# Performance work log

Measured on AMD Instinct MI355X. Metric: run time of the kernel, lower is better.

Reference implementation:

```python
import jax, jax.numpy as jnp
import numpy as np

N_QUBITS = 16
BATCH = 512
NUM_CLASSES = 100


def _rx_mat(theta):
    """RX matrix; theta shape (...,) -> (..., 2, 2) complex64."""
    c = jnp.cos(theta / 2).astype(jnp.complex64)
    s = (-1j * jnp.sin(theta / 2)).astype(jnp.complex64)
    row0 = jnp.stack([c, s], axis=-1)
    row1 = jnp.stack([s, c], axis=-1)
    return jnp.stack([row0, row1], axis=-2)


def _rot_mat(phi, theta, omega):
    """qml.Rot = RZ(omega) RY(theta) RZ(phi); scalars/arrays -> (..., 2, 2)."""
    c = jnp.cos(theta / 2)
    s = jnp.sin(theta / 2)
    e_m = jnp.exp(-0.5j * (phi + omega).astype(jnp.complex64))
    e_p = jnp.exp(0.5j * (phi + omega).astype(jnp.complex64))
    e_dm = jnp.exp(-0.5j * (phi - omega).astype(jnp.complex64))
    e_dp = jnp.exp(0.5j * (phi - omega).astype(jnp.complex64))
    row0 = jnp.stack([e_m * c, -e_dp * s], axis=-1)
    row1 = jnp.stack([e_dm * s, e_p * c], axis=-1)
    return jnp.stack([row0, row1], axis=-2).astype(jnp.complex64)


def _apply_1q(state, U, w):
    """Apply shared (2,2) gate U on wire w. state: (B,) + (2,)*16."""
    s = jnp.moveaxis(state, w + 1, -1)
    s = jnp.einsum('ij,...j->...i', U, s)
    return jnp.moveaxis(s, -1, w + 1)


def _apply_1q_batched(state, U, w):
    """Apply per-sample (B,2,2) gate on wire w."""
    s = jnp.moveaxis(state, w + 1, -1)
    s = jnp.einsum('bij,b...j->b...i', U, s)
    return jnp.moveaxis(s, -1, w + 1)


def _apply_crx(state, theta, ctrl, tgt):
    """Controlled-RX(theta) with control ctrl, target tgt (shared scalar theta)."""
    U = _rx_mat(theta)
    s = jnp.moveaxis(state, (ctrl + 1, tgt + 1), (-2, -1))
    s1 = jnp.einsum('ij,...j->...i', U, s[..., 1, :])
    s = jnp.stack([s[..., 0, :], s1], axis=-2)
    return jnp.moveaxis(s, (-2, -1), (ctrl + 1, tgt + 1))


def _circuit(x, rot_l1, crx_l1, rot_l2, crx_l2):
    B = x.shape[0]
    # |0...0> initial state, shape (B, 2, 2, ..., 2)
    state = jnp.zeros((B,) + (2,) * N_QUBITS, dtype=jnp.complex64)
    state = state.at[(slice(None),) + (0,) * N_QUBITS].set(1.0)

    for layer_rot, layer_crx in ((rot_l1, crx_l1), (rot_l2, crx_l2)):
        # AngleEmbedding: RX(x[:, i]) on wire i (per-sample angles)
        for i in range(N_QUBITS):
            state = _apply_1q_batched(state, _rx_mat(x[:, i]), i)
        # Rot gates
        for i in range(N_QUBITS):
            U = _rot_mat(layer_rot[i, 0], layer_rot[i, 1], layer_rot[i, 2])
            state = _apply_1q(state, U, i)
        # ring CRX
        for i in range(N_QUBITS):
            state = _apply_crx(state, layer_crx[i, 0], i, (i + 1) % N_QUBITS)

    # <Z_i> = P(bit_i = 0) - P(bit_i = 1)
    probs = state.real ** 2 + state.imag ** 2  # (B,) + (2,)*16
    expvals = []
    for i in range(N_QUBITS):
        axes = tuple(a for a in range(1, N_QUBITS + 1) if a != i + 1)
        marg = probs.sum(axis=axes)  # (B, 2)
        expvals.append(marg[:, 0] - marg[:, 1])
    return jnp.stack(expvals, axis=1).astype(jnp.float32)  # (B, 16)


def setup_inputs() -> dict:
    key = jax.random.key(0)
    ks = jax.random.split(key, 7)
    return {
        'x': jax.random.normal(ks[0], (BATCH, N_QUBITS), jnp.float32),
        'rot_l1': jax.random.normal(ks[1], (N_QUBITS, 3), jnp.float32),
        'crx_l1': jax.random.normal(ks[2], (N_QUBITS, 1), jnp.float32),
        'rot_l2': jax.random.normal(ks[3], (N_QUBITS, 3), jnp.float32),
        'crx_l2': jax.random.normal(ks[4], (N_QUBITS, 1), jnp.float32),
        'W': jax.random.normal(ks[5], (NUM_CLASSES, N_QUBITS), jnp.float32) * 0.25,
        'b': jax.random.normal(ks[6], (NUM_CLASSES,), jnp.float32) * 0.01,
    }


def reference(x, rot_l1, crx_l1, rot_l2, crx_l2, W, b):
    feats = _circuit(x, rot_l1, crx_l1, rot_l2, crx_l2)  # (B, 16)
    logits = feats @ W.T + b  # (B, num_classes)
    return jax.nn.log_softmax(logits, axis=1)
```

## Files before the change

### kernel.cpp

```cpp
#include <hip/hip_runtime.h>
#include <math.h>

#define NQ 16
#define NBATCH 512
#define NCLS 100

typedef float v2f __attribute__((ext_vector_type(2)));
typedef __fp16 f16x2 __attribute__((ext_vector_type(2)));
typedef _Float16 half8 __attribute__((ext_vector_type(8)));
typedef float f32x4 __attribute__((ext_vector_type(4)));

__device__ __forceinline__ v2f mkv(float x, float y){ v2f r; r.x = x; r.y = y; return r; }
__device__ __forceinline__ f16x2 pack_h(v2f a){ return __builtin_amdgcn_cvt_pkrtz(a.x, a.y); }
__device__ __forceinline__ f16x2 pack_h2(float a, float b){ return __builtin_amdgcn_cvt_pkrtz(a, b); }
__device__ __forceinline__ v2f unpack_h(f16x2 h){ return mkv((float)h.x, (float)h.y); }

union pack16 { f16x2 h[4]; uint4 u; };

__device__ __forceinline__ v2f pk_cmul(v2f a, v2f b){
  v2f t, d;
  asm("v_pk_mul_f32 %0, %1, %2 op_sel:[0,0] op_sel_hi:[1,0]"
      : "=v"(t) : "v"(a), "v"(b));
  asm("v_pk_fma_f32 %0, %1, %2, %3 op_sel:[1,1,0] op_sel_hi:[0,1,1] neg_lo:[1,0,0]"
      : "=v"(d) : "v"(a), "v"(b), "v"(t));
  return d;
}
__device__ __forceinline__ v2f pk_cmul_acc(v2f a, v2f b, v2f acc){
  v2f t, d;
  asm("v_pk_fma_f32 %0, %1, %2, %3 op_sel:[0,0,0] op_sel_hi:[1,0,1]"
      : "=v"(t) : "v"(a), "v"(b), "v"(acc));
  asm("v_pk_fma_f32 %0, %1, %2, %3 op_sel:[1,1,0] op_sel_hi:[0,1,1] neg_lo:[1,0,0]"
      : "=v"(d) : "v"(a), "v"(b), "v"(t));
  return d;
}
__device__ __forceinline__ void pk_rx(v2f &a, v2f &b, v2f cs){
  v2f t1, t2, na, nb;
  asm("v_pk_mul_f32 %0, %1, %2 op_sel:[0,0] op_sel_hi:[0,1]"
      : "=v"(t1) : "v"(cs), "v"(a));
  asm("v_pk_mul_f32 %0, %1, %2 op_sel:[0,0] op_sel_hi:[0,1]"
      : "=v"(t2) : "v"(cs), "v"(b));
  asm("v_pk_fma_f32 %0, %1, %2, %3 op_sel:[1,1,0] op_sel_hi:[1,0,1] neg_hi:[0,1,0]"
      : "=v"(na) : "v"(cs), "v"(b), "v"(t1));
  asm("v_pk_fma_f32 %0, %1, %2, %3 op_sel:[1,1,0] op_sel_hi:[1,0,1] neg_hi:[0,1,0]"
      : "=v"(nb) : "v"(cs), "v"(a), "v"(t2));
  a = na; b = nb;
}

template<int MT>
__device__ __forceinline__ void crx_pred(v2f (&v)[16], bool on, v2f cs){
  v2f id = mkv(1.f, 0.f);
  v2f cs_p = on ? cs : id;
  #pragma unroll
  for (int r=0;r<16;r++) if(!(r&MT)) pk_rx(v[r], v[r|MT], cs_p);
}
template<int MT>
__device__ __forceinline__ void crx_on(v2f (&v)[16], v2f cs){
  #pragma unroll
  for (int r=0;r<16;r++) if(!(r&MT)) pk_rx(v[r], v[r|MT], cs);
}
template<int MC,int MT>
__device__ __forceinline__ void crx_rr(v2f (&v)[16], v2f cs){
  #pragma unroll
  for (int r=0;r<16;r++) if((r&MC)&&!(r&MT)) pk_rx(v[r], v[r|MT], cs);
}
template<int M>
__device__ __forceinline__ void reg_gate(v2f (&v)[16], v2f u00, v2f u01, v2f u10, v2f u11){
  #pragma unroll
  for (int r=0;r<16;r++) if(!(r&M)){
    v2f a = v[r], b = v[r|M];
    v[r]   = pk_cmul_acc(u01, b, pk_cmul(u00, a));
    v[r|M] = pk_cmul_acc(u11, b, pk_cmul(u10, a));
  }
}
__device__ __forceinline__ void build_rxw(v2f cs, v2f w00, v2f w01, v2f w10, v2f w11,
      v2f &f00, v2f &f01, v2f &f10, v2f &f11){
  f00 = w00; f10 = w10; pk_rx(f00, f10, cs);
  f01 = w01; f11 = w11; pk_rx(f01, f11, cs);
}

__device__ __forceinline__ int lds_phys(int c){ return c ^ (((c>>4)^(c>>8))&15); }
__device__ __forceinline__ int swz(int m, int q){
  return m*4 + (q ^ (m&3) ^ ((m>>2)&3));
}
__device__ __forceinline__ int oswz(int idx){ return idx ^ ((idx>>5)&31); }

__global__ __launch_bounds__(256) void kprep(const float* __restrict__ x,
      const float* __restrict__ rot1, const float* __restrict__ crx1,
      const float* __restrict__ rot2, const float* __restrict__ crx2,
      v2f* __restrict__ fU, v2f* __restrict__ cm)
{
  int t = blockIdx.x*blockDim.x + threadIdx.x;
  if (t < 2*NBATCH*NQ){
    int w  = t & 15;
    int bb = (t>>4) & (NBATCH-1);
    int L  = t >> 13;
    const float* rot = L ? rot2 : rot1;
    float phi = rot[w*3+0], th = rot[w*3+1], om = rot[w*3+2];
    float ct = cosf(0.5f*th), stt = sinf(0.5f*th);
    float a1 = 0.5f*(phi+om), a2 = 0.5f*(phi-om);
    float emx = cosf(a1), emy = -sinf(a1);
    float epx = cosf(a1), epy =  sinf(a1);
    float edmx = cosf(a2), edmy = -sinf(a2);
    float edpx = cosf(a2), edpy =  sinf(a2);
    float R00x = emx*ct,   R00y = emy*ct;
    float R01x = -edpx*stt, R01y = -edpy*stt;
    float R10x = edmx*stt, R10y = edmy*stt;
    float R11x = epx*ct,   R11y = epy*ct;
    float xv = x[bb*NQ + w];
    float cx = cosf(0.5f*xv), sx = sinf(0.5f*xv);
    v2f* o = fU + (size_t)t*4;
    o[0] = mkv(R00x*cx + R01y*sx,  R00y*cx - R01x*sx);
    o[1] = mkv(R00y*sx + R01x*cx, -R00x*sx + R01y*cx);
    o[2] = mkv(R10x*cx + R11y*sx,  R10y*cx - R11x*sx);
    o[3] = mkv(R10y*sx + R11x*cx, -R10x*sx + R11y*cx);
  }
  if (t < 2*NQ){
    int L = t>>4, w = t&15;
    const float* cxl = L ? crx2 : crx1;
    float thc = cxl[w];
    cm[t] = mkv(cosf(0.5f*thc), sinf(0.5f*thc));
  }
}

__global__ __launch_bounds__(256) void kprep2(const v2f* __restrict__ fU,
      const v2f* __restrict__ cm, v2f* __restrict__ Tbl)
{
  int t = blockIdx.x*blockDim.x + threadIdx.x;
  if (t >= 2*NBATCH) return;
  int bb = t >> 1, bit = t & 1;
  const v2f* U = fU + (size_t)bb*64;
  v2f p[16];
  p[0] = U[48]; p[1] = U[50];
  p[2] = pk_cmul(p[0], U[54]); p[3] = pk_cmul(p[1], U[54]);
  p[0] = pk_cmul(p[0], U[52]); p[1] = pk_cmul(p[1], U[52]);
  #pragma unroll
  for (int i=0;i<4;i++){ p[i+4]=pk_cmul(p[i],U[58]); p[i]=pk_cmul(p[i],U[56]); }
  #pragma unroll
  for (int i=0;i<8;i++){ p[i+8]=pk_cmul(p[i],U[62]); p[i]=pk_cmul(p[i],U[60]); }
  if (bit){
    #pragma unroll
    for (int r=0;r<16;r++) if(!(r&1)) pk_rx(p[r], p[r|1], cm[11]);
  }
  #pragma unroll
  for (int r=0;r<16;r++) if((r&1)&&!(r&2)) pk_rx(p[r], p[r|2], cm[12]);
  #pragma unroll
  for (int r=0;r<16;r++) if((r&2)&&!(r&4)) pk_rx(p[r], p[r|4], cm[13]);
  #pragma unroll
  for (int r=0;r<16;r++) if((r&4)&&!(r&8)) pk_rx(p[r], p[r|8], cm[14]);
  v2f* o = Tbl + ((size_t)bb<<5) + (bit<<4);
  #pragma unroll
  for (int r=0;r<16;r++) o[r] = p[r];
}

__device__ __forceinline__ void store_Bfrag(_Float16* Bt16, size_t hb, int r0, const v2f (&v)[16]){
  int k0 = 2*r0;
  int lk = 16*(k0>>3);
  int j0 = k0 & 7;
  #pragma unroll
  for (int n=0;n<16;n++){
    _Float16 re  = (_Float16)v[n].x;
    _Float16 im  = (_Float16)v[n].y;
    _Float16 nim = (_Float16)(-v[n].y);
    size_t ln = (size_t)(lk + n);
    Bt16[((hb+0)*64 + ln)*8 + j0]   = re;
    Bt16[((hb+0)*64 + ln)*8 + j0+1] = nim;
    Bt16[((hb+1)*64 + ln)*8 + j0]   = im;
    Bt16[((hb+1)*64 + ln)*8 + j0+1] = re;
  }
}

__global__ __launch_bounds__(256) void kprepG(const v2f* __restrict__ fU2,
      const v2f* __restrict__ cm2, _Float16* __restrict__ Bt16)
{
  int t = blockIdx.x*blockDim.x + threadIdx.x;
  if (t >= NBATCH*2*2*16) return;
  int r0 = t & 15;
  int var = (t>>4) & 1;
  int stage = (t>>5) & 1;
  int bg = t >> 6;
  const v2f* U2 = fU2 + ((size_t)bg<<6);
  v2f v[16];
  #pragma unroll
  for (int r=0;r<16;r++) v[r] = mkv(0.f,0.f);
  v[r0] = mkv(1.f,0.f);
  if (stage == 0){
    reg_gate<1>(v, U2[28],U2[29],U2[30],U2[31]);
    reg_gate<2>(v, U2[32],U2[33],U2[34],U2[35]);
    reg_gate<4>(v, U2[36],U2[37],U2[38],U2[39]);
    reg_gate<8>(v, U2[40],U2[41],U2[42],U2[43]);
    if (var) crx_on<1>(v, cm2[6]);
    crx_rr<1,2>(v, cm2[7]);
    crx_rr<2,4>(v, cm2[8]);
    crx_rr<4,8>(v, cm2[9]);
  } else {
    reg_gate<1>(v, U2[44],U2[45],U2[46],U2[47]);
    reg_gate<2>(v, U2[48],U2[49],U2[50],U2[51]);
    reg_gate<4>(v, U2[52],U2[53],U2[54],U2[55]);
    reg_gate<8>(v, U2[56],U2[57],U2[58],U2[59]);
    if (var) crx_on<1>(v, cm2[10]);
    crx_rr<1,2>(v, cm2[11]);
    crx_rr<2,4>(v, cm2[12]);
    crx_rr<4,8>(v, cm2[13]);
  }
  size_t hb = (((size_t)bg*2 + stage)*2 + var)*2;
  store_Bfrag(Bt16, hb, r0, v);
}

__global__ __launch_bounds__(256) void kprepG2(const v2f* __restrict__ fU2,
      const v2f* __restrict__ cm1, const v2f* __restrict__ cm2,
      _Float16* __restrict__ Bt16)
{
  int t = blockIdx.x*blockDim.x + threadIdx.x;
  if (t >= NBATCH*2*2*16) return;
  int r0 = t & 15;
  int var = (t>>4) & 1;
  int stage = (t>>5) & 1;
  int bg = t >> 6;
  const v2f* U2 = fU2 + ((size_t)bg<<6);
  v2f v[16];
  #pragma unroll
  for (int r=0;r<16;r++) v[r] = mkv(0.f,0.f);
  v[r0] = mkv(1.f,0.f);
  if (stage == 0){
    if (var) crx_on<1>(v, cm1[15]);
    reg_gate<1>(v, U2[0], U2[1], U2[2], U2[3]);
    reg_gate<2>(v, U2[4], U2[5], U2[6], U2[7]);
    reg_gate<4>(v, U2[8], U2[9], U2[10],U2[11]);
    reg_gate<8>(v, U2[12],U2[13],U2[14],U2[15]);
    crx_rr<1,2>(v, cm2[0]);
    crx_rr<2,4>(v, cm2[1]);
    crx_rr<4,8>(v, cm2[2]);
  } else {
    reg_gate<1>(v, U2[16],U2[17],U2[18],U2[19]);
    reg_gate<2>(v, U2[20],U2[21],U2[22],U2[23]);
    reg_gate<4>(v, U2[24],U2[25],U2[26],U2[27]);
    if (var) crx_on<1>(v, cm2[3]);
    crx_rr<1,2>(v, cm2[4]);
    crx_rr<2,4>(v, cm2[5]);
  }
  size_t hb = (((size_t)bg*2 + stage)*2 + var)*2;
  store_Bfrag(Bt16, hb, r0, v);
}

__global__ __launch_bounds__(256) void kpass1(const v2f* __restrict__ fU1,
      const v2f* __restrict__ cm1, f16x2* __restrict__ compact)
{
  int lane = threadIdx.x & 63;
  int wv = threadIdx.x >> 6;
  int bg = blockIdx.x;
  const v2f* U = fU1 + ((size_t)bg<<6);
  v2f a = (lane&1) ? U[2] : U[0];
  a = pk_cmul(a, ((lane>>1)&1) ? U[22] : U[20]);
  a = pk_cmul(a, ((lane>>2)&1) ? U[26] : U[24]);
  a = pk_cmul(a, ((lane>>3)&1) ? U[30] : U[28]);
  a = pk_cmul(a, ((lane>>4)&1) ? U[34] : U[32]);
  a = pk_cmul(a, ((lane>>5)&1) ? U[38] : U[36]);
  a = pk_cmul(a, (wv&1) ? U[42] : U[40]);
  a = pk_cmul(a, ((wv>>1)&1) ? U[46] : U[44]);
  v2f v[16];
  v[0] = pk_cmul(a, U[4]);    v[1] = pk_cmul(a, U[6]);
  v[2] = pk_cmul(v[0], U[10]); v[3] = pk_cmul(v[1], U[10]);
  v[0] = pk_cmul(v[0], U[8]);  v[1] = pk_cmul(v[1], U[8]);
  #pragma unroll
  for (int i=0;i<4;i++){ v[i+4]=pk_cmul(v[i],U[14]); v[i]=pk_cmul(v[i],U[12]); }
  #pragma unroll
  for (int i=0;i<8;i++){ v[i+8]=pk_cmul(v[i],U[18]); v[i]=pk_cmul(v[i],U[16]); }
  crx_pred<1>(v, (lane&1)!=0, cm1[0]);
  crx_rr<1,2>(v, cm1[1]);
  crx_rr<2,4>(v, cm1[2]);
  crx_rr<4,8>(v, cm1[3]);
  __shared__ v2f lds[4096];
  #pragma unroll
  for (int r=0;r<16;r++){
    int c = (lane&1) | (r<<1) | (((lane>>1)&31)<<5) | (wv<<10);
    lds[lds_phys(c)] = v[r];
  }
  __syncthreads();
  #pragma unroll
  for (int r=0;r<16;r++){
    int c = ((lane>>1)&15) | ((lane&1)<<4) | (r<<5) | (((lane>>5)&1)<<9) | (wv<<10);
    v[r] = lds[lds_phys(c)];
  }
  crx_pred<1>(v, (lane&1)!=0, cm1[4]);
  crx_rr<1,2>(v, cm1[5]);
  crx_rr<2,4>(v, cm1[6]);
  crx_rr<4,8>(v, cm1[7]);
  __syncthreads();
  #pragma unroll
  for (int r=0;r<16;r++){
    int c = ((lane>>1)&15) | ((lane&1)<<4) | (r<<5) | (((lane>>5)&1)<<9) | (wv<<10);
    lds[lds_phys(c)] = v[r];
  }
  __syncthreads();
  #pragma unroll
  for (int r=0;r<16;r++){
    int c = (lane&63) | (wv<<6) | (((r>>3)&1)<<8) | ((r&7)<<9);
    v[r] = lds[lds_phys(c)];
  }
  crx_rr<8,1>(v, cm1[8]);
  crx_rr<1,2>(v, cm1[9]);
  crx_rr<2,4>(v, cm1[10]);
  __syncthreads();
  #pragma unroll
  for (int r=0;r<16;r++){
    int c = (lane&63) | (wv<<6) | (((r>>3)&1)<<8) | ((r&7)<<9);
    lds[lds_phys(c)] = v[r];
  }
  __syncthreads();
  f16x2* outp = compact + ((size_t)bg<<12);
  #pragma unroll
  for (int r=0;r<16;r++){
    int c = ((lane>>1)&31) | (wv<<5) | (r<<7) | ((lane&1)<<11);
    outp[lane | (wv<<6) | (r<<8)] = pack_h(lds[lds_phys(c)]);
  }
}

__global__ __launch_bounds__(256) void kpass2(const f16x2* __restrict__ compact,
      const v2f* __restrict__ Tbl, const half8* __restrict__ Btab2,
      f16x2* __restrict__ st, int b0)
{
  int lane = threadIdx.x & 63;
  int wv = threadIdx.x >> 6;
  int blk = blockIdx.x;
  int bl = blk >> 4, h = blk & 15;
  int bg = b0 + bl;
  __shared__ uint4 lbufA[1024];
  __shared__ uint4 lbufB[1024];
  f16x2* lbufH = (f16x2*)lbufA;

  v2f a = unpack_h(compact[((size_t)bg<<12) | (size_t)(lane | (wv<<6) | (h<<8))]);
  const v2f* T = Tbl + ((size_t)bg<<5) + ((lane&1)<<4);
  int sel = wv & 1;
  size_t hb1 = (((size_t)bg*2 + 0)*2 + sel)*2;
  size_t hb2 = (((size_t)bg*2 + 1)*2 + sel)*2;
  half8 B1a = Btab2[(hb1+0)*64 + lane];
  half8 B2a = Btab2[(hb1+1)*64 + lane];
  half8 B1b = Btab2[(hb2+0)*64 + lane];
  half8 B2b = Btab2[(hb2+1)*64 + lane];
  f32x4 zz = {0.f, 0.f, 0.f, 0.f};

  int kb = (lane>>1) & 15;
  int mA_fix = (lane&1) | ((lane>>5)<<4) | ((wv&1)<<5) | ((wv>>1)<<7);
  #pragma unroll
  for (int r=0;r<16;r++){
    v2f val = pk_cmul(a, T[r]);
    int m = mA_fix | ((r&7)<<1) | ((r>>3)<<6);
    lbufH[swz(m, kb>>2)*4 + (kb&3)] = pack_h(val);
  }
  __syncthreads();

  f32x4 dre[4], dim[4];
  #pragma unroll
  for (int t=0;t<4;t++){
    int m = (wv<<6) | (t<<4) | (lane&15);
    half8 af = *(const half8*)&lbufA[swz(m, lane>>4)];
    dre[t] = __builtin_amdgcn_mfma_f32_16x16x32_f16(af, B1a, zz, 0, 0, 0);
    dim[t] = __builtin_amdgcn_mfma_f32_16x16x32_f16(af, B2a, zz, 0, 0, 0);
  }
  int n = lane & 15, lq = lane >> 4;
  int q_c = ((wv>>1)&1) | ((n&1)<<1);
  #pragma unroll
  for (int reg=0;reg<4;reg++){
    int mC = (lq&1) | (((n>>1)&1)<<1) | (((n>>2)&1)<<2) | ((lq>>1)<<3)
           | ((reg&1)<<4) | (((reg>>1)&1)<<5) | (((n>>3)&1)<<6) | ((wv&1)<<7);
    pack16 pk;
    #pragma unroll
    for (int t=0;t<4;t++) pk.h[t] = pack_h2(dre[t][reg], dim[t][reg]);
    lbufB[swz(mC, q_c)] = pk.u;
  }
  __syncthreads();

  #pragma unroll
  for (int t2=0;t2<4;t2++){
    int m = (wv<<6) | (t2<<4) | (lane&15);
    half8 af = *(const half8*)&lbufB[swz(m, lane>>4)];
    f32x4 ere = __builtin_amdgcn_mfma_f32_16x16x32_f16(af, B1b, zz, 0, 0, 0);
    f32x4 eim = __builtin_amdgcn_mfma_f32_16x16x32_f16(af, B2b, zz, 0, 0, 0);
    #pragma unroll
    for (int reg=0;reg<4;reg++){
      int idx = ((lane>>3)&1) | (((reg>>1)&1)<<1) | ((t2&1)<<2) | (((t2>>1)&1)<<3)
              | ((reg&1)<<4) | ((wv&1)<<5) | (((lane>>4)&1)<<6) | (((lane>>5)&1)<<7)
              | ((lane&1)<<8) | (((lane>>1)&1)<<9) | (((lane>>2)&1)<<10) | (((wv>>1)&1)<<11);
      lbufH[oswz(idx)] = pack_h2(ere[reg], eim[reg]);
    }
  }
  __syncthreads();

  f16x2* S = st + ((size_t)bl<<16);
  #pragma unroll
  for (int r=0;r<16;r++){
    int idx = lane | (wv<<6) | (r<<8);
    S[idx | (h<<12)] = lbufH[oswz(idx)];
  }
}

__global__ __launch_bounds__(256) void kpass3(const f16x2* __restrict__ st,
      const v2f* __restrict__ fU2, const v2f* __restrict__ cm2,
      const half8* __restrict__ Btab,
      float* __restrict__ expv, int b0)
{
  int lane = threadIdx.x & 63;
  int wv = threadIdx.x >> 6;
  int blk = blockIdx.x;
  int bl = blk >> 4, h = blk & 15;
  int bg = b0 + bl;
  const f16x2* S = st + ((size_t)bl<<16);
  const v2f* U2 = fU2 + ((size_t)bg<<6);
  __shared__ uint4 lbufA[1024];
  __shared__ uint4 lbufB[1024];

  int abase = (((h>>1)&1)<<5) | ((h&1)<<6) | (((h>>2)&1)<<8) | (((h>>3)&1)<<9)
            | ((wv&1)<<10) | (((wv>>1)&1)<<11);
  f16x2 v[16];
  #pragma unroll
  for (int r=0;r<16;r++){
    v[r] = S[(lane&31) | (((lane>>5)&1)<<7) | abase | (r<<12)];
  }
  int m1 = ((lane>>2)&15) | (((wv>>1)&1)<<4) | ((lane&1)<<5)
         | ((wv&1)<<6) | (((lane>>1)&1)<<7);
  #pragma unroll
  for (int q=0;q<4;q++){
    pack16 pk;
    pk.h[0]=v[4*q]; pk.h[1]=v[4*q+1]; pk.h[2]=v[4*q+2]; pk.h[3]=v[4*q+3];
    lbufA[swz(m1,q)] = pk.u;
  }

  int sel = wv & 1;
  size_t hb1 = (((size_t)bg*2 + 0)*2 + sel)*2;
  size_t hb2 = (((size_t)bg*2 + 1)*2 + sel)*2;
  half8 B1a = Btab[(hb1+0)*64 + lane];
  half8 B2a = Btab[(hb1+1)*64 + lane];
  half8 B1b = Btab[(hb2+0)*64 + lane];
  half8 B2b = Btab[(hb2+1)*64 + lane];
  f32x4 zz = {0.f, 0.f, 0.f, 0.f};

  __syncthreads();

  {
    int n = lane & 15;
    int q2 = lane >> 4;
    #pragma unroll
    for (int t=0;t<4;t++){
      int m = (wv<<6) | (t<<4) | (lane&15);
      half8 af = *(const half8*)&lbufA[swz(m, lane>>4)];
      f32x4 dre = __builtin_amdgcn_mfma_f32_16x16x32_f16(af, B1a, zz, 0, 0, 0);
      f32x4 dim = __builtin_amdgcn_mfma_f32_16x16x32_f16(af, B2a, zz, 0, 0, 0);
      int m2 = t | ((n&7)<<2) | (((wv>>1)&1)<<5) | (((n>>3)&1)<<6) | ((wv&1)<<7);
      pack16 pk;
      #pragma unroll
      for (int rg=0;rg<4;rg++) pk.h[rg] = pack_h2(dre[rg], dim[rg]);
      lbufB[swz(m2, q2)] = pk.u;
    }
  }
  __syncthreads();

  v2f G00, G01, G10, G11;
  {
    v2f g00=U2[60], g01=U2[61], g10=U2[62], g11=U2[63];
    v2f f00,f01,f10,f11;
    build_rxw(cm2[14], g00,g01,g10,g11, f00,f01,f10,f11);
    bool on3 = ((lane>>3)&1) != 0;
    G00 = on3?f00:g00; G01 = on3?f01:g01; G10 = on3?f10:g10; G11 = on3?f11:g11;
  }
  float tot=0.f, S15=0.f, S0w=0.f, S9=0.f, S1w=0.f;
  #pragma unroll
  for (int t2=0;t2<4;t2++){
    int m = (wv<<6) | (t2<<4) | (lane&15);
    half8 af = *(const half8*)&lbufB[swz(m, lane>>4)];
    f32x4 ere = __builtin_amdgcn_mfma_f32_16x16x32_f16(af, B1b, zz, 0, 0, 0);
    f32x4 eim = __builtin_amdgcn_mfma_f32_16x16x32_f16(af, B2b, zz, 0, 0, 0);
    v2f a0 = mkv(ere[0], eim[0]);
    v2f a1 = mkv(ere[1], eim[1]);
    v2f a2 = mkv(ere[2], eim[2]);
    v2f a3 = mkv(ere[3], eim[3]);
    v2f n0 = pk_cmul_acc(G01, a1, pk_cmul(G00, a0));
    v2f n1 = pk_cmul_acc(G11, a1, pk_cmul(G10, a0));
    v2f n2 = pk_cmul_acc(G01, a3, pk_cmul(G00, a2));
    v2f n3 = pk_cmul_acc(G11, a3, pk_cmul(G10, a2));
    pk_rx(n1, n3, cm2[15]);
    float p0 = n0.x*n0.x + n0.y*n0.y;
    float p1 = n1.x*n1.x + n1.y*n1.y;
    float p2 = n2.x*n2.x + n2.y*n2.y;
    float p3 = n3.x*n3.x + n3.y*n3.y;
    float ps = p0+p1+p2+p3;
    tot += ps;
    S15 += p1+p3;
    S0w += p2+p3;
    if (t2&1) S9 += ps;
    if (t2&2) S1w += ps;
  }
  float s = tot;
  float u[6];
  #pragma unroll
  for (int b=0;b<6;b++){
    int m = 1<<b;
    float tt = __shfl_xor(s, m, 64);
    u[b] = s - tt;
    s = s + tt;
    #pragma unroll
    for (int j=0;j<6;j++) if (j<b) u[j] += __shfl_xor(u[j], m, 64);
  }
  #pragma unroll
  for (int d=1; d<64; d<<=1){
    S15 += __shfl_xor(S15, d, 64);
    S0w += __shfl_xor(S0w, d, 64);
    S9  += __shfl_xor(S9, d, 64);
    S1w += __shfl_xor(S1w, d, 64);
  }
  __syncthreads();
  float* ef = (float*)lbufA;
  if (lane==0){
    ef[wv*16+11]=u[0]; ef[wv*16+12]=u[1]; ef[wv*16+13]=u[2]; ef[wv*16+14]=u[3];
    ef[wv*16+7]=u[4];  ef[wv*16+8]=u[5];
    ef[wv*16+15]=s-2.f*S15; ef[wv*16+0]=s-2.f*S0w;
    ef[wv*16+9]=s-2.f*S9;   ef[wv*16+1]=s-2.f*S1w;
    ef[wv*16+10]=(wv&1)?-s:s; ef[wv*16+6]=(wv&2)?-s:s;
    ef[wv*16+2]=(h&1)?-s:s; ef[wv*16+3]=(h&2)?-s:s;
    ef[wv*16+4]=(h&4)?-s:s; ef[wv*16+5]=(h&8)?-s:s;
  }
  __syncthreads();
  if (threadIdx.x < 16){
    float r4 = ef[threadIdx.x]+ef[16+threadIdx.x]+ef[32+threadIdx.x]+ef[48+threadIdx.x];
    atomicAdd(expv + (size_t)bg*NQ + threadIdx.x, r4);
  }
}

__global__ __launch_bounds__(128) void klogits(const float* __restrict__ expv,
      const float* __restrict__ W, const float* __restrict__ bias,
      float* __restrict__ out)
{
  int b = blockIdx.x;
  int tid = threadIdx.x;
  __shared__ float f[NQ];
  __shared__ float lg[NCLS];
  if (tid < NQ) f[tid] = expv[b*NQ + tid];
  __syncthreads();
  if (tid < NCLS){
    float acc = bias[tid];
    #pragma unroll
    for (int i=0;i<NQ;i++) acc += f[i]*W[tid*NQ+i];
    lg[tid] = acc;
  }
  __syncthreads();
  if (tid < NCLS){
    float m = -1e30f;
    for (int i=0;i<NCLS;i++) m = fmaxf(m, lg[i]);
    float sum = 0.f;
    for (int i=0;i<NCLS;i++) sum += expf(lg[i]-m);
    out[b*NCLS+tid] = lg[tid] - m - logf(sum);
  }
}

extern "C" void kernel_launch(void* const* d_in, const int* in_sizes, int n_in,
                              void* d_out, int out_size, void* d_ws, size_t ws_size,
                              hipStream_t stream)
{
  const float* x    = (const float*)d_in[0];
  const float* rot1 = (const float*)d_in[1];
  const float* crx1 = (const float*)d_in[2];
  const float* rot2 = (const float*)d_in[3];
  const float* crx2 = (const float*)d_in[4];
  const float* W    = (const float*)d_in[5];
  const float* bias = (const float*)d_in[6];
  float* out = (float*)d_out;

  char* ws = (char*)d_ws;
  float* expv = (float*)ws;
  v2f*   fU   = (v2f*)(ws + (40<<10));
  v2f*   cmm  = (v2f*)(ws + (560<<10));
  v2f*   Tbl  = (v2f*)(ws + (564<<10));
  _Float16* Bt16  = (_Float16*)(ws + (704<<10));
  _Float16* Bt16b = (_Float16*)(ws + (4800<<10));
  f16x2* compact = (f16x2*)(ws + (8896<<10));
  const size_t stOff = (size_t)(8896<<10) + ((size_t)NBATCH<<14);
  f16x2* st   = (f16x2*)(ws + stOff);

  hipMemsetAsync(expv, 0, NBATCH*NQ*sizeof(float), stream);
  kprep<<<(2*NBATCH*NQ + 255)/256, 256, 0, stream>>>(x, rot1, crx1, rot2, crx2, fU, cmm);

  v2f* fU1 = fU;
  v2f* fU2 = fU + 32768;
  v2f* cm1 = cmm;
  v2f* cm2 = cmm + 16;

  kprep2<<<(2*NBATCH + 255)/256, 256, 0, stream>>>(fU1, cm1, Tbl);
  kprepG<<<(NBATCH*2*2*16 + 255)/256, 256, 0, stream>>>(fU2, cm2, Bt16);
  kprepG2<<<(NBATCH*2*2*16 + 255)/256, 256, 0, stream>>>(fU2, cm1, cm2, Bt16b);
  kpass1<<<NBATCH, 256, 0, stream>>>(fU1, cm1, compact);

  size_t avail = (ws_size > stOff) ? (ws_size - stOff) : 0;
  int chunk = NBATCH;
  while (chunk > 1 && (size_t)chunk*65536*sizeof(f16x2) > avail) chunk >>= 1;

  for (int b0 = 0; b0 < NBATCH; b0 += chunk){
    kpass2<<<chunk*16, 256, 0, stream>>>(compact, Tbl, (const half8*)Bt16b, st, b0);
    kpass3<<<chunk*16, 256, 0, stream>>>(st, fU2, cm2, (const half8*)Bt16, expv, b0);
  }
  klogits<<<NBATCH, 128, 0, stream>>>(expv, W, bias, out);
}
```

Before: 117.6 us.

## Merge gate-prep kernels, halve LDS in pass kernels, defer B-fragment loads

```diff
diff --git a/kernel.cpp b/kernel.cpp
--- a/kernel.cpp
+++ b/kernel.cpp
@@ -31,6 +31,12 @@
       : "=v"(t) : "v"(a), "v"(b), "v"(acc));
   asm("v_pk_fma_f32 %0, %1, %2, %3 op_sel:[1,1,0] op_sel_hi:[0,1,1] neg_lo:[1,0,0]"
       : "=v"(d) : "v"(a), "v"(b), "v"(t));
+  return d;
+}
+__device__ __forceinline__ v2f pk_fma_el(v2f a, v2f b, v2f c){
+  v2f d;
+  asm("v_pk_fma_f32 %0, %1, %2, %3"
+      : "=v"(d) : "v"(a), "v"(b), "v"(c));
   return d;
 }
 __device__ __forceinline__ void pk_rx(v2f &a, v2f &b, v2f cs){
@@ -169,11 +175,13 @@
   }
 }
 
-__global__ __launch_bounds__(256) void kprepG(const v2f* __restrict__ fU2,
-      const v2f* __restrict__ cm2, _Float16* __restrict__ Bt16)
-{
-  int t = blockIdx.x*blockDim.x + threadIdx.x;
-  if (t >= NBATCH*2*2*16) return;
+__global__ __launch_bounds__(256) void kprepGall(const v2f* __restrict__ fU2,
+      const v2f* __restrict__ cm1, const v2f* __restrict__ cm2,
+      _Float16* __restrict__ Bt16, _Float16* __restrict__ Bt16b)
+{
+  int tt = blockIdx.x*blockDim.x + threadIdx.x;
+  int which = tt >> 15;
+  int t = tt & 32767;
   int r0 = t & 15;
   int var = (t>>4) & 1;
   int stage = (t>>5) & 1;
@@ -183,63 +191,49 @@
   #pragma unroll
   for (int r=0;r<16;r++) v[r] = mkv(0.f,0.f);
   v[r0] = mkv(1.f,0.f);
-  if (stage == 0){
-    reg_gate<1>(v, U2[28],U2[29],U2[30],U2[31]);
-    reg_gate<2>(v, U2[32],U2[33],U2[34],U2[35]);
-    reg_gate<4>(v, U2[36],U2[37],U2[38],U2[39]);
-    reg_gate<8>(v, U2[40],U2[41],U2[42],U2[43]);
-    if (var) crx_on<1>(v, cm2[6]);
-    crx_rr<1,2>(v, cm2[7]);
-    crx_rr<2,4>(v, cm2[8]);
-    crx_rr<4,8>(v, cm2[9]);
+  if (which == 0){
+    if (stage == 0){
+      reg_gate<1>(v, U2[28],U2[29],U2[30],U2[31]);
+      reg_gate<2>(v, U2[32],U2[33],U2[34],U2[35]);
+      reg_gate<4>(v, U2[36],U2[37],U2[38],U2[39]);
+      reg_gate<8>(v, U2[40],U2[41],U2[42],U2[43]);
+      if (var) crx_on<1>(v, cm2[6]);
+      crx_rr<1,2>(v, cm2[7]);
+      crx_rr<2,4>(v, cm2[8]);
+      crx_rr<4,8>(v, cm2[9]);
+    } else {
+      reg_gate<1>(v, U2[44],U2[45],U2[46],U2[47]);
+      reg_gate<2>(v, U2[48],U2[49],U2[50],U2[51]);
+      reg_gate<4>(v, U2[52],U2[53],U2[54],U2[55]);
+      reg_gate<8>(v, U2[56],U2[57],U2[58],U2[59]);
+      if (var) crx_on<1>(v, cm2[10]);
+      crx_rr<1,2>(v, cm2[11]);
+      crx_rr<2,4>(v, cm2[12]);
+      crx_rr<4,8>(v, cm2[13]);
+    }
+    size_t hb = (((size_t)bg*2 + stage)*2 + var)*2;
+    store_Bfrag(Bt16, hb, r0, v);
   } else {
-    reg_gate<1>(v, U2[44],U2[45],U2[46],U2[47]);
-    reg_gate<2>(v, U2[48],U2[49],U2[50],U2[51]);
-    reg_gate<4>(v, U2[52],U2[53],U2[54],U2[55]);
-    reg_gate<8>(v, U2[56],U2[57],U2[58],U2[59]);
-    if (var) crx_on<1>(v, cm2[10]);
-    crx_rr<1,2>(v, cm2[11]);
-    crx_rr<2,4>(v, cm2[12]);
-    crx_rr<4,8>(v, cm2[13]);
-  }
-  size_t hb = (((size_t)bg*2 + stage)*2 + var)*2;
-  store_Bfrag(Bt16, hb, r0, v);
-}
-
-__global__ __launch_bounds__(256) void kprepG2(const v2f* __restrict__ fU2,
-      const v2f* __restrict__ cm1, const v2f* __restrict__ cm2,
-      _Float16* __restrict__ Bt16)
-{
-  int t = blockIdx.x*blockDim.x + threadIdx.x;
-  if (t >= NBATCH*2*2*16) return;
-  int r0 = t & 15;
-  int var = (t>>4) & 1;
-  int stage = (t>>5) & 1;
-  int bg = t >> 6;
-  const v2f* U2 = fU2 + ((size_t)bg<<6);
-  v2f v[16];
-  #pragma unroll
-  for (int r=0;r<16;r++) v[r] = mkv(0.f,0.f);
-  v[r0] = mkv(1.f,0.f);
-  if (stage == 0){
-    if (var) crx_on<1>(v, cm1[15]);
-    reg_gate<1>(v, U2[0], U2[1], U2[2], U2[3]);
-    reg_gate<2>(v, U2[4], U2[5], U2[6], U2[7]);
-    reg_gate<4>(v, U2[8], U2[9], U2[10],U2[11]);
-    reg_gate<8>(v, U2[12],U2[13],U2[14],U2[15]);
-    crx_rr<1,2>(v, cm2[0]);
-    crx_rr<2,4>(v, cm2[1]);
-    crx_rr<4,8>(v, cm2[2]);
-  } else {
-    reg_gate<1>(v, U2[16],U2[17],U2[18],U2[19]);
-    reg_gate<2>(v, U2[20],U2[21],U2[22],U2[23]);
-    reg_gate<4>(v, U2[24],U2[25],U2[26],U2[27]);
-    if (var) crx_on<1>(v, cm2[3]);
-    crx_rr<1,2>(v, cm2[4]);
-    crx_rr<2,4>(v, cm2[5]);
-  }
-  size_t hb = (((size_t)bg*2 + stage)*2 + var)*2;
-  store_Bfrag(Bt16, hb, r0, v);
+    if (stage == 0){
+      if (var) crx_on<1>(v, cm1[15]);
+      reg_gate<1>(v, U2[0], U2[1], U2[2], U2[3]);
+      reg_gate<2>(v, U2[4], U2[5], U2[6], U2[7]);
+      reg_gate<4>(v, U2[8], U2[9], U2[10],U2[11]);
+      reg_gate<8>(v, U2[12],U2[13],U2[14],U2[15]);
+      crx_rr<1,2>(v, cm2[0]);
+      crx_rr<2,4>(v, cm2[1]);
+      crx_rr<4,8>(v, cm2[2]);
+    } else {
+      reg_gate<1>(v, U2[16],U2[17],U2[18],U2[19]);
+      reg_gate<2>(v, U2[20],U2[21],U2[22],U2[23]);
+      reg_gate<4>(v, U2[24],U2[25],U2[26],U2[27]);
+      if (var) crx_on<1>(v, cm2[3]);
+      crx_rr<1,2>(v, cm2[4]);
+      crx_rr<2,4>(v, cm2[5]);
+    }
+    size_t hb = (((size_t)bg*2 + stage)*2 + var)*2;
+    store_Bfrag(Bt16b, hb, r0, v);
+  }
 }
 
 __global__ __launch_bounds__(256) void kpass1(const v2f* __restrict__ fU1,
@@ -324,9 +318,8 @@
   int blk = blockIdx.x;
   int bl = blk >> 4, h = blk & 15;
   int bg = b0 + bl;
-  __shared__ uint4 lbufA[1024];
-  __shared__ uint4 lbufB[1024];
-  f16x2* lbufH = (f16x2*)lbufA;
+  __shared__ uint4 lbuf[1024];
+  f16x2* lbufH = (f16x2*)lbuf;
 
   v2f a = unpack_h(compact[((size_t)bg<<12) | (size_t)(lane | (wv<<6) | (h<<8))]);
   const v2f* T = Tbl + ((size_t)bg<<5) + ((lane&1)<<4);
@@ -335,8 +328,6 @@
   size_t hb2 = (((size_t)bg*2 + 1)*2 + sel)*2;
   half8 B1a = Btab2[(hb1+0)*64 + lane];
   half8 B2a = Btab2[(hb1+1)*64 + lane];
-  half8 B1b = Btab2[(hb2+0)*64 + lane];
-  half8 B2b = Btab2[(hb2+1)*64 + lane];
   f32x4 zz = {0.f, 0.f, 0.f, 0.f};
 
   int kb = (lane>>1) & 15;
@@ -348,12 +339,18 @@
     lbufH[swz(m, kb>>2)*4 + (kb&3)] = pack_h(val);
   }
   __syncthreads();
-
-  f32x4 dre[4], dim[4];
+  uint4 af1[4];
   #pragma unroll
   for (int t=0;t<4;t++){
     int m = (wv<<6) | (t<<4) | (lane&15);
-    half8 af = *(const half8*)&lbufA[swz(m, lane>>4)];
+    af1[t] = lbuf[swz(m, lane>>4)];
+  }
+  __syncthreads();
+
+  f32x4 dre[4], dim[4];
+  #pragma unroll
+  for (int t=0;t<4;t++){
+    half8 af = *(const half8*)&af1[t];
     dre[t] = __builtin_amdgcn_mfma_f32_16x16x32_f16(af, B1a, zz, 0, 0, 0);
     dim[t] = __builtin_amdgcn_mfma_f32_16x16x32_f16(af, B2a, zz, 0, 0, 0);
   }
@@ -366,14 +363,22 @@
     pack16 pk;
     #pragma unroll
     for (int t=0;t<4;t++) pk.h[t] = pack_h2(dre[t][reg], dim[t][reg]);
-    lbufB[swz(mC, q_c)] = pk.u;
-  }
-  __syncthreads();
-
+    lbuf[swz(mC, q_c)] = pk.u;
+  }
+  __syncthreads();
+  uint4 af2[4];
   #pragma unroll
   for (int t2=0;t2<4;t2++){
     int m = (wv<<6) | (t2<<4) | (lane&15);
-    half8 af = *(const half8*)&lbufB[swz(m, lane>>4)];
+    af2[t2] = lbuf[swz(m, lane>>4)];
+  }
+  __syncthreads();
+
+  half8 B1b = Btab2[(hb2+0)*64 + lane];
+  half8 B2b = Btab2[(hb2+1)*64 + lane];
+  #pragma unroll
+  for (int t2=0;t2<4;t2++){
+    half8 af = *(const half8*)&af2[t2];
     f32x4 ere = __builtin_amdgcn_mfma_f32_16x16x32_f16(af, B1b, zz, 0, 0, 0);
     f32x4 eim = __builtin_amdgcn_mfma_f32_16x16x32_f16(af, B2b, zz, 0, 0, 0);
     #pragma unroll
@@ -406,8 +411,7 @@
   int bg = b0 + bl;
   const f16x2* S = st + ((size_t)bl<<16);
   const v2f* U2 = fU2 + ((size_t)bg<<6);
-  __shared__ uint4 lbufA[1024];
-  __shared__ uint4 lbufB[1024];
+  __shared__ uint4 lbuf[1024];
 
   int abase = (((h>>1)&1)<<5) | ((h&1)<<6) | (((h>>2)&1)<<8) | (((h>>3)&1)<<9)
             | ((wv&1)<<10) | (((wv>>1)&1)<<11);
@@ -422,18 +426,21 @@
   for (int q=0;q<4;q++){
     pack16 pk;
     pk.h[0]=v[4*q]; pk.h[1]=v[4*q+1]; pk.h[2]=v[4*q+2]; pk.h[3]=v[4*q+3];
-    lbufA[swz(m1,q)] = pk.u;
-  }
-
+    lbuf[swz(m1,q)] = pk.u;
+  }
   int sel = wv & 1;
   size_t hb1 = (((size_t)bg*2 + 0)*2 + sel)*2;
   size_t hb2 = (((size_t)bg*2 + 1)*2 + sel)*2;
   half8 B1a = Btab[(hb1+0)*64 + lane];
   half8 B2a = Btab[(hb1+1)*64 + lane];
-  half8 B1b = Btab[(hb2+0)*64 + lane];
-  half8 B2b = Btab[(hb2+1)*64 + lane];
   f32x4 zz = {0.f, 0.f, 0.f, 0.f};
-
+  __syncthreads();
+  uint4 af1[4];
+  #pragma unroll
+  for (int t=0;t<4;t++){
+    int m = (wv<<6) | (t<<4) | (lane&15);
+    af1[t] = lbuf[swz(m, lane>>4)];
+  }
   __syncthreads();
 
   {
@@ -441,19 +448,26 @@
     int q2 = lane >> 4;
     #pragma unroll
     for (int t=0;t<4;t++){
-      int m = (wv<<6) | (t<<4) | (lane&15);
-      half8 af = *(const half8*)&lbufA[swz(m, lane>>4)];
+      half8 af = *(const half8*)&af1[t];
       f32x4 dre = __builtin_amdgcn_mfma_f32_16x16x32_f16(af, B1a, zz, 0, 0, 0);
       f32x4 dim = __builtin_amdgcn_mfma_f32_16x16x32_f16(af, B2a, zz, 0, 0, 0);
       int m2 = t | ((n&7)<<2) | (((wv>>1)&1)<<5) | (((n>>3)&1)<<6) | ((wv&1)<<7);
       pack16 pk;
       #pragma unroll
       for (int rg=0;rg<4;rg++) pk.h[rg] = pack_h2(dre[rg], dim[rg]);
-      lbufB[swz(m2, q2)] = pk.u;
+      lbuf[swz(m2, q2)] = pk.u;
     }
   }
   __syncthreads();
-
+  uint4 af2[4];
+  #pragma unroll
+  for (int t2=0;t2<4;t2++){
+    int m = (wv<<6) | (t2<<4) | (lane&15);
+    af2[t2] = lbuf[swz(m, lane>>4)];
+  }
+
+  half8 B1b = Btab[(hb2+0)*64 + lane];
+  half8 B2b = Btab[(hb2+1)*64 + lane];
   v2f G00, G01, G10, G11;
   {
     v2f g00=U2[60], g01=U2[61], g10=U2[62], g11=U2[63];
@@ -462,11 +476,11 @@
     bool on3 = ((lane>>3)&1) != 0;
     G00 = on3?f00:g00; G01 = on3?f01:g01; G10 = on3?f10:g10; G11 = on3?f11:g11;
   }
-  float tot=0.f, S15=0.f, S0w=0.f, S9=0.f, S1w=0.f;
+  v2f accT = mkv(0.f,0.f), acc15 = mkv(0.f,0.f), acc0 = mkv(0.f,0.f);
+  v2f acc9 = mkv(0.f,0.f), acc1 = mkv(0.f,0.f);
   #pragma unroll
   for (int t2=0;t2<4;t2++){
-    int m = (wv<<6) | (t2<<4) | (lane&15);
-    half8 af = *(const half8*)&lbufB[swz(m, lane>>4)];
+    half8 af = *(const half8*)&af2[t2];
     f32x4 ere = __builtin_amdgcn_mfma_f32_16x16x32_f16(af, B1b, zz, 0, 0, 0);
     f32x4 eim = __builtin_amdgcn_mfma_f32_16x16x32_f16(af, B2b, zz, 0, 0, 0);
     v2f a0 = mkv(ere[0], eim[0]);
@@ -478,17 +492,22 @@
     v2f n2 = pk_cmul_acc(G01, a3, pk_cmul(G00, a2));
     v2f n3 = pk_cmul_acc(G11, a3, pk_cmul(G10, a2));
     pk_rx(n1, n3, cm2[15]);
-    float p0 = n0.x*n0.x + n0.y*n0.y;
-    float p1 = n1.x*n1.x + n1.y*n1.y;
-    float p2 = n2.x*n2.x + n2.y*n2.y;
-    float p3 = n3.x*n3.x + n3.y*n3.y;
-    float ps = p0+p1+p2+p3;
-    tot += ps;
-    S15 += p1+p3;
-    S0w += p2+p3;
-    if (t2&1) S9 += ps;
-    if (t2&2) S1w += ps;
-  }
+    v2f q0 = pk_fma_el(n0,n0,mkv(0,0));
+    v2f q1 = pk_fma_el(n1,n1,mkv(0,0));
+    v2f q2v = pk_fma_el(n2,n2,mkv(0,0));
+    v2f q3 = pk_fma_el(n3,n3,mkv(0,0));
+    v2f qs = q0+q1+q2v+q3;
+    accT += qs;
+    acc15 += q1+q3;
+    acc0  += q2v+q3;
+    if (t2&1) acc9 += qs;
+    if (t2&2) acc1 += qs;
+  }
+  float tot = accT.x + accT.y;
+  float S15 = acc15.x + acc15.y;
+  float S0w = acc0.x + acc0.y;
+  float S9  = acc9.x + acc9.y;
+  float S1w = acc1.x + acc1.y;
   float s = tot;
   float u[6];
   #pragma unroll
@@ -508,7 +527,7 @@
     S1w += __shfl_xor(S1w, d, 64);
   }
   __syncthreads();
-  float* ef = (float*)lbufA;
+  float* ef = (float*)lbuf;
   if (lane==0){
     ef[wv*16+11]=u[0]; ef[wv*16+12]=u[1]; ef[wv*16+13]=u[2]; ef[wv*16+14]=u[3];
     ef[wv*16+7]=u[4];  ef[wv*16+8]=u[5];
@@ -584,8 +603,7 @@
   v2f* cm2 = cmm + 16;
 
   kprep2<<<(2*NBATCH + 255)/256, 256, 0, stream>>>(fU1, cm1, Tbl);
-  kprepG<<<(NBATCH*2*2*16 + 255)/256, 256, 0, stream>>>(fU2, cm2, Bt16);
-  kprepG2<<<(NBATCH*2*2*16 + 255)/256, 256, 0, stream>>>(fU2, cm1, cm2, Bt16b);
+  kprepGall<<<(2*NBATCH*2*2*16 + 255)/256, 256, 0, stream>>>(fU2, cm1, cm2, Bt16, Bt16b);
   kpass1<<<NBATCH, 256, 0, stream>>>(fU1, cm1, compact);
 
   size_t avail = (ws_size > stOff) ? (ws_size - stOff) : 0;
```

Result: faster. 113.0 us (-3.9%).
